# Kernel tuning notes

Hardware: AMD Instinct MI355X
Metric: run time of the kernel (lower is better)

The kernel has to match this reference:

```python
import jax, jax.numpy as jnp
import numpy as np

N_NODES = 50000


def _gcn_conv(x, edge_index, W, b):
    # PyG GCNConv (default flags): add self-loops, symmetric normalization,
    # linear transform, scatter-add aggregation, bias.
    N = x.shape[0]
    row, col = edge_index[0], edge_index[1]  # messages flow row -> col
    loop = jnp.arange(N)
    row_f = jnp.concatenate([row, loop])
    col_f = jnp.concatenate([col, loop])
    deg = jax.ops.segment_sum(jnp.ones(col_f.shape[0], dtype=x.dtype), col_f,
                              num_segments=N)
    deg_inv_sqrt = jnp.where(deg > 0, jax.lax.rsqrt(jnp.maximum(deg, 1e-12)), 0.0)
    norm = deg_inv_sqrt[row_f] * deg_inv_sqrt[col_f]  # [E+N]
    h = x @ W                                          # [N, out]
    msg = h[row_f] * norm[:, None]                     # gather + scale
    out = jax.ops.segment_sum(msg, col_f, num_segments=N)  # scatter-add
    return out + b


def setup_inputs() -> dict:
    key = jax.random.key(0)
    ks = jax.random.split(key, 6)
    d_in, d_hid, d_out = 128, 128, 64
    E = 800000
    x = jax.random.normal(ks[0], (N_NODES, d_in), dtype=jnp.float32)
    edge_index = jax.random.randint(ks[1], (2, E), 0, N_NODES, dtype=jnp.int64)
    edge_label = jax.random.uniform(ks[2], (100000,), dtype=jnp.float32)
    edge_label_index = jax.random.randint(ks[3], (2, 100000), 0, N_NODES,
                                          dtype=jnp.int64)
    # Glorot-style init for GCNConv linear weights
    W1 = jax.random.normal(ks[4], (d_in, d_hid), dtype=jnp.float32) / np.sqrt(d_in)
    b1 = jnp.zeros((d_hid,), dtype=jnp.float32)
    W2 = jax.random.normal(ks[5], (d_hid, d_out), dtype=jnp.float32) / np.sqrt(d_hid)
    b2 = jnp.zeros((d_out,), dtype=jnp.float32)
    return {"x": x, "edge_index": edge_index, "edge_label": edge_label,
            "edge_label_index": edge_label_index,
            "W1": W1, "b1": b1, "W2": W2, "b2": b2}


def reference(x, edge_index, edge_label, edge_label_index, W1, b1, W2, b2):
    h = jax.nn.relu(_gcn_conv(x, edge_index, W1, b1))
    # dropout is identity in eval mode (training=False)
    z = _gcn_conv(h, edge_index, W2, b2)
    return z
```

## Files before the change

### kernel.cpp

```cpp
#include <hip/hip_runtime.h>


typedef unsigned int u32;
typedef unsigned short ushort;
typedef __attribute__((ext_vector_type(8))) short short8;
typedef __attribute__((ext_vector_type(8))) unsigned short us8;
typedef __attribute__((ext_vector_type(4))) float floatx4;

static inline int cdiv_l(long a, int b) { return (int)((a + b - 1) / b); }

constexpr int NPB  = 512;
constexpr int EPB  = 4096;
constexpr int MAXB = 128;
constexpr int CAP  = 12288;

__device__ __forceinline__ u32 pack_bf16(float a, float b) {
  union { float f; u32 i; } ua, ub;
  ua.f = a; ub.f = b;
  u32 x = (ua.i + 0x7fffu + ((ua.i >> 16) & 1u)) >> 16;
  u32 y = (ub.i + 0x7fffu + ((ub.i >> 16) & 1u)) & 0xffff0000u;
  return x | y;
}

__device__ __forceinline__ short bf16r(float f) {
  union { float f; u32 i; } u; u.f = f;
  return (short)((u.i + 0x7fffu + ((u.i >> 16) & 1u)) >> 16);
}

__device__ __forceinline__ void dq8(float* a, uint2 v, float sd) {
  a[0] += (float)(v.x & 255u) * sd;
  a[1] += (float)((v.x >> 8) & 255u) * sd;
  a[2] += (float)((v.x >> 16) & 255u) * sd;
  a[3] += (float)(v.x >> 24) * sd;
  a[4] += (float)(v.y & 255u) * sd;
  a[5] += (float)((v.y >> 8) & 255u) * sd;
  a[6] += (float)((v.y >> 16) & 255u) * sd;
  a[7] += (float)(v.y >> 24) * sd;
}

__global__ __launch_bounds__(256) void k_pack(
    const float* __restrict__ W1, const float* __restrict__ W2,
    u32* __restrict__ w1f, u32* __restrict__ w2f, int* __restrict__ cur) {
  const int tid = threadIdx.x;
  const int b = blockIdx.x;
  if (b == 0 && tid < MAXB) cur[tid] = 0;
  if (b < 8) {
    const int s = b * 256 + tid;
    const int lane = s & 63, frag = s >> 6;
    const int kc = frag >> 3, cb = frag & 7;
    const float* src =
        W1 + (long)(kc * 32 + (lane >> 4) * 8) * 128 + cb * 16 + (lane & 15);
    u32 o[4];
#pragma unroll
    for (int p = 0; p < 4; ++p)
      o[p] = pack_bf16(src[(2 * p) * 128], src[(2 * p + 1) * 128]);
    *(uint4*)(w1f + (long)s * 4) = make_uint4(o[0], o[1], o[2], o[3]);
  } else {
    const int s = (b - 8) * 256 + tid;
    const int lane = s & 63, frag = s >> 6;
    const int kc = frag >> 2, cb = frag & 3;
    const float* src =
        W2 + (long)(kc * 32 + (lane >> 4) * 8) * 64 + cb * 16 + (lane & 15);
    u32 o[4];
#pragma unroll
    for (int p = 0; p < 4; ++p)
      o[p] = pack_bf16(src[(2 * p) * 64], src[(2 * p + 1) * 64]);
    *(uint4*)(w2f + (long)s * 4) = make_uint4(o[0], o[1], o[2], o[3]);
  }
}

__global__ __launch_bounds__(256) void k_fused1(
    const int* __restrict__ ei, int* __restrict__ cur, u32* __restrict__ ebuf,
    int E, int NBE,
    const float* __restrict__ x, const u32* __restrict__ w1f,
    u32* __restrict__ h8, float* __restrict__ scale, int N) {
  __shared__ float eb[4][16 * 133];
  const int tid = threadIdx.x;

  if (blockIdx.x < (unsigned)NBE) {
    u32* ecache = (u32*)&eb[0][0];
    int* hist   = (int*)&eb[2][0];
    int* curs   = hist + MAXB;
    const int* ecol = ei + E;
    if (tid < MAXB) hist[tid] = 0;
    __syncthreads();
    const int base = blockIdx.x * EPB;
#pragma unroll
    for (int j = 0; j < EPB / 256; ++j) {
      int e = base + j * 256 + tid;
      u32 pk = 0xffffffffu;
      if (e < E) {
        u32 r = (u32)ei[e];
        u32 c = (u32)ecol[e];
        pk = r | (c << 16);
        atomicAdd(hist + (c >> 9), 1);
      }
      ecache[j * 256 + tid] = pk;
    }
    __syncthreads();
    if (tid < MAXB) {
      int n = hist[tid];
      curs[tid] = tid * CAP + (n ? atomicAdd(cur + tid, n) : 0);
    }
    __syncthreads();
#pragma unroll
    for (int j = 0; j < EPB / 256; ++j) {
      u32 pk = ecache[j * 256 + tid];
      if (pk != 0xffffffffu) {
        u32 c = pk >> 16;
        int b = c >> 9;
        int p = atomicAdd(curs + b, 1);
        if (p < (b + 1) * CAP)
          ebuf[p] = (pk & 0xffffu) | ((c & (NPB - 1)) << 16);
      }
    }
    return;
  }

  constexpr int K = 128, NC = 8, LROW = 133;
  const int w = tid >> 6, lane = tid & 63;
  const int quad = lane >> 4, n16 = lane & 15;
  const int row0 = ((blockIdx.x - NBE) * 4 + w) * 16;

  floatx4 acc[NC];
#pragma unroll
  for (int c = 0; c < NC; ++c) acc[c] = {0.f, 0.f, 0.f, 0.f};

  const int am = row0 + n16;
  const bool av = am < N;
  const float* arow = x + (long)am * K;
  const short8* wf = (const short8*)w1f;

#pragma unroll
  for (int kc = 0; kc < 4; ++kc) {
    const int kb = kc * 32 + quad * 8;
    float4 a0 = make_float4(0.f, 0.f, 0.f, 0.f);
    float4 a1 = make_float4(0.f, 0.f, 0.f, 0.f);
    if (av) {
      a0 = *(const float4*)(arow + kb);
      a1 = *(const float4*)(arow + kb + 4);
    }
    short8 af;
    af[0] = bf16r(a0.x); af[1] = bf16r(a0.y); af[2] = bf16r(a0.z); af[3] = bf16r(a0.w);
    af[4] = bf16r(a1.x); af[5] = bf16r(a1.y); af[6] = bf16r(a1.z); af[7] = bf16r(a1.w);
#pragma unroll
    for (int c = 0; c < NC; ++c) {
      short8 bf = wf[(kc * 8 + c) * 64 + lane];
      acc[c] = __builtin_amdgcn_mfma_f32_16x16x32_bf16(af, bf, acc[c], 0, 0, 0);
    }
  }

  float* ep = eb[w];
#pragma unroll
  for (int c = 0; c < NC; ++c)
#pragma unroll
    for (int r = 0; r < 4; ++r)
      ep[(quad * 4 + r) * LROW + c * 16 + n16] = acc[c][r];
  __syncthreads();

  const int rr = lane >> 2, seg = lane & 3;
  const float* rowp = ep + rr * LROW + seg * 32;
  float m = 0.f;
#pragma unroll
  for (int c = 0; c < 32; ++c) m = fmaxf(m, fabsf(rowp[c]));
  m = fmaxf(m, __shfl_xor(m, 1, 4));
  m = fmaxf(m, __shfl_xor(m, 2, 4));
  const float inv = (m > 0.f) ? 127.f / m : 0.f;
  const float s = m / 127.f;
  u32 q[8];
#pragma unroll
  for (int wd = 0; wd < 8; ++wd) {
    u32 b0 = (u32)((int)rintf(rowp[wd * 4 + 0] * inv) + 128);
    u32 b1 = (u32)((int)rintf(rowp[wd * 4 + 1] * inv) + 128);
    u32 b2 = (u32)((int)rintf(rowp[wd * 4 + 2] * inv) + 128);
    u32 b3 = (u32)((int)rintf(rowp[wd * 4 + 3] * inv) + 128);
    q[wd] = (b0 & 255u) | ((b1 & 255u) << 8) | ((b2 & 255u) << 16) | (b3 << 24);
  }
  const int rg = row0 + rr;
  if (rg < N) {
    uint4* dst = (uint4*)(h8 + (long)rg * 32 + seg * 8);
    dst[0] = make_uint4(q[0], q[1], q[2], q[3]);
    dst[1] = make_uint4(q[4], q[5], q[6], q[7]);
    if (seg == 0) scale[rg] = s;
  }
}

__global__ __launch_bounds__(NPB) void k_csr(const u32* __restrict__ ebuf,
                                             const int* __restrict__ cur,
                                             const float* __restrict__ scale,
                                             int* __restrict__ off,
                                             int* __restrict__ deg,
                                             float* __restrict__ dis,
                                             float* __restrict__ sd,
                                             ushort* __restrict__ csr, int N) {
  __shared__ int cnt[NPB];
  __shared__ int curl[NPB];
  __shared__ int wsum[NPB / 64];
  const int tid = threadIdx.x;
  const int b = blockIdx.x;
  const int s = b * CAP;
  const int e = s + min(cur[b], CAP);
  cnt[tid] = 0;
  __syncthreads();
  for (int i = s + tid; i < e; i += NPB)
    atomicAdd(cnt + (ebuf[i] >> 16), 1);
  __syncthreads();
  const int lane = tid & 63, w = tid >> 6;
  const int v = cnt[tid];
  const int vp = (v + 7) & ~7;
  int incl = vp;
#pragma unroll
  for (int d = 1; d < 64; d <<= 1) {
    int x = __shfl_up(incl, d, 64);
    if (lane >= d) incl += x;
  }
  if (lane == 63) wsum[w] = incl;
  __syncthreads();
  if (w == 0 && lane < NPB / 64) {
    int sv = wsum[lane];
#pragma unroll
    for (int d = 1; d < NPB / 64; d <<= 1) {
      int x = __shfl_up(sv, d, 64);
      if (lane >= d) sv += x;
    }
    wsum[lane] = sv;
  }
  __syncthreads();
  int excl = ((w > 0) ? wsum[w - 1] : 0) + incl - vp;
  int node = b * NPB + tid;
  if (node < N) {
    float dv = rsqrtf((float)v + 1.0f);
    off[node] = s + excl;
    deg[node] = v;
    dis[node] = dv;
    sd[node] = scale[node] * dv;
  }
  curl[tid] = excl;
  __syncthreads();
  for (int i = s + tid; i < e; i += NPB) {
    u32 pk = ebuf[i];
    int p = atomicAdd(curl + (pk >> 16), 1);
    csr[s + p] = (ushort)(pk & 0xffffu);
  }
}

__global__ __launch_bounds__(256) void k_gg(
    const uint2* __restrict__ h8, const int* __restrict__ off,
    const int* __restrict__ deg, const ushort* __restrict__ csr,
    const float* __restrict__ dis, const float* __restrict__ sd,
    const float* __restrict__ b1, const u32* __restrict__ w2f,
    u32* __restrict__ h2, float* __restrict__ s2, int N) {
  constexpr int LG = 65;
  constexpr int LC = 66;
  __shared__ u32 lg[16 * LG];
  __shared__ float cb[16 * LC];
  const int tid = threadIdx.x;
  const int r = tid >> 4;
  const int lf = tid & 15;
  const int row0 = blockIdx.x * 16;
  const int n = row0 + r;

  u32 gw[4] = {0, 0, 0, 0};
  if (n < N) {
    const int s = off[n], e = s + deg[n];
    const float dn = dis[n];
    float acc[8] = {};
    float K = 0.f;
    {
      float sn = sd[n];
      dq8(acc, h8[(long)n * 16 + lf], sn);
      K += sn;
    }
    int j = s;
    for (; j + 8 <= e; j += 8) {
      us8 ev = *(const us8*)(csr + j);
      const int i0 = ev[0], i1 = ev[1], i2 = ev[2], i3 = ev[3];
      const int i4 = ev[4], i5 = ev[5], i6 = ev[6], i7 = ev[7];
      const float d0 = sd[i0], d1 = sd[i1], d2 = sd[i2], d3 = sd[i3];
      const float d4 = sd[i4], d5 = sd[i5], d6 = sd[i6], d7 = sd[i7];
      uint2 v0 = h8[(long)i0 * 16 + lf];
      uint2 v1 = h8[(long)i1 * 16 + lf];
      uint2 v2 = h8[(long)i2 * 16 + lf];
      uint2 v3 = h8[(long)i3 * 16 + lf];
      uint2 v4 = h8[(long)i4 * 16 + lf];
      uint2 v5 = h8[(long)i5 * 16 + lf];
      uint2 v6 = h8[(long)i6 * 16 + lf];
      uint2 v7 = h8[(long)i7 * 16 + lf];
      dq8(acc, v0, d0); dq8(acc, v1, d1); dq8(acc, v2, d2); dq8(acc, v3, d3);
      dq8(acc, v4, d4); dq8(acc, v5, d5); dq8(acc, v6, d6); dq8(acc, v7, d7);
      K += ((d0 + d1) + (d2 + d3)) + ((d4 + d5) + (d6 + d7));
    }
    if (j < e) {
      us8 ev = *(const us8*)(csr + j);
#pragma unroll
      for (int t = 0; t < 8; ++t) {
        if (j + t < e) {
          const int it = ev[t];
          const float dt = sd[it];
          dq8(acc, h8[(long)it * 16 + lf], dt);
          K += dt;
        }
      }
    }
    const int f8 = lf * 8;
    const float4 bv0 = *(const float4*)(b1 + f8);
    const float4 bv1 = *(const float4*)(b1 + f8 + 4);
    const float bb[8] = {bv0.x, bv0.y, bv0.z, bv0.w, bv1.x, bv1.y, bv1.z, bv1.w};
    const float kc = 128.f * K;
#pragma unroll
    for (int q = 0; q < 8; ++q)
      acc[q] = fmaxf((acc[q] - kc) * dn + bb[q], 0.f);
#pragma unroll
    for (int q = 0; q < 4; ++q)
      gw[q] = pack_bf16(acc[2 * q], acc[2 * q + 1]);
  }
#pragma unroll
  for (int q = 0; q < 4; ++q) lg[r * LG + lf * 4 + q] = gw[q];
  __syncthreads();

  const int w = tid >> 6, lane = tid & 63;
  const int quad = lane >> 4, n16 = lane & 15;
  floatx4 acc4 = {0.f, 0.f, 0.f, 0.f};
#pragma unroll
  for (int kc = 0; kc < 4; ++kc) {
    const int kb = kc * 32 + quad * 8;
    const u32* ap = &lg[n16 * LG + (kb >> 1)];
    u32 aw[4] = {ap[0], ap[1], ap[2], ap[3]};
    short8 af = *(short8*)aw;
    short8 bf = ((const short8*)w2f)[(kc * 4 + w) * 64 + lane];
    acc4 = __builtin_amdgcn_mfma_f32_16x16x32_bf16(af, bf, acc4, 0, 0, 0);
  }
  float dd[4];
#pragma unroll
  for (int r4 = 0; r4 < 4; ++r4) {
    int rg = row0 + quad * 4 + r4;
    dd[r4] = (rg < N) ? dis[rg] : 0.f;
  }
#pragma unroll
  for (int r4 = 0; r4 < 4; ++r4)
    cb[(quad * 4 + r4) * LC + w * 16 + n16] = acc4[r4] * dd[r4];
  __syncthreads();

  const int rr2 = tid >> 4, lf2 = tid & 15;
  const float* rp = cb + rr2 * LC + lf2 * 4;
  float mx = fmaxf(fmaxf(fabsf(rp[0]), fabsf(rp[1])),
                   fmaxf(fabsf(rp[2]), fabsf(rp[3])));
  mx = fmaxf(mx, __shfl_xor(mx, 1, 16));
  mx = fmaxf(mx, __shfl_xor(mx, 2, 16));
  mx = fmaxf(mx, __shfl_xor(mx, 4, 16));
  mx = fmaxf(mx, __shfl_xor(mx, 8, 16));
  const float inv2 = (mx > 0.f) ? 127.f / mx : 0.f;
  const int rg2 = row0 + rr2;
  if (rg2 < N) {
    u32 q0 = (u32)((int)rintf(rp[0] * inv2) + 128);
    u32 q1 = (u32)((int)rintf(rp[1] * inv2) + 128);
    u32 q2 = (u32)((int)rintf(rp[2] * inv2) + 128);
    u32 q3 = (u32)((int)rintf(rp[3] * inv2) + 128);
    h2[(long)rg2 * 16 + lf2] =
        (q0 & 255u) | ((q1 & 255u) << 8) | ((q2 & 255u) << 16) | (q3 << 24);
    if (lf2 == 0) s2[rg2] = mx / 127.f;
  }
}

__global__ __launch_bounds__(256) void k_gather2(
    const uint2* __restrict__ hs, const int* __restrict__ off,
    const int* __restrict__ deg, const ushort* __restrict__ csr,
    const float* __restrict__ dis, const float* __restrict__ sc2,
    const float* __restrict__ bias, float* __restrict__ out, int N) {
  constexpr int L = 8;
  const int local = threadIdx.x / L;
  const int lf = threadIdx.x % L;
  const int n = blockIdx.x * (256 / L) + local;
  if (n >= N) return;
  const int s = off[n], e = s + deg[n];
  float acc[8] = {};
  float K = 0.f;
  {
    float t0 = sc2[n];
    dq8(acc, hs[(long)n * L + lf], t0);
    K += t0;
  }
  int j = s;
  for (; j + 8 <= e; j += 8) {
    us8 ev = *(const us8*)(csr + j);
    const int i0 = ev[0], i1 = ev[1], i2 = ev[2], i3 = ev[3];
    const int i4 = ev[4], i5 = ev[5], i6 = ev[6], i7 = ev[7];
    const float d0 = sc2[i0], d1 = sc2[i1], d2 = sc2[i2], d3 = sc2[i3];
    const float d4 = sc2[i4], d5 = sc2[i5], d6 = sc2[i6], d7 = sc2[i7];
    uint2 v0 = hs[(long)i0 * L + lf];
    uint2 v1 = hs[(long)i1 * L + lf];
    uint2 v2 = hs[(long)i2 * L + lf];
    uint2 v3 = hs[(long)i3 * L + lf];
    uint2 v4 = hs[(long)i4 * L + lf];
    uint2 v5 = hs[(long)i5 * L + lf];
    uint2 v6 = hs[(long)i6 * L + lf];
    uint2 v7 = hs[(long)i7 * L + lf];
    dq8(acc, v0, d0); dq8(acc, v1, d1); dq8(acc, v2, d2); dq8(acc, v3, d3);
    dq8(acc, v4, d4); dq8(acc, v5, d5); dq8(acc, v6, d6); dq8(acc, v7, d7);
    K += ((d0 + d1) + (d2 + d3)) + ((d4 + d5) + (d6 + d7));
  }
  if (j < e) {
    us8 ev = *(const us8*)(csr + j);
#pragma unroll
    for (int t = 0; t < 8; ++t) {
      if (j + t < e) {
        const int it = ev[t];
        const float dt = sc2[it];
        dq8(acc, hs[(long)it * L + lf], dt);
        K += dt;
      }
    }
  }
  const float d = dis[n];
  const float kc = 128.f * K;
  const int f8 = lf * 8;
  const float4 b0 = *(const float4*)(bias + f8);
  const float4 b1v = *(const float4*)(bias + f8 + 4);
  float4 o0, o1;
  o0.x = (acc[0] - kc) * d + b0.x;
  o0.y = (acc[1] - kc) * d + b0.y;
  o0.z = (acc[2] - kc) * d + b0.z;
  o0.w = (acc[3] - kc) * d + b0.w;
  o1.x = (acc[4] - kc) * d + b1v.x;
  o1.y = (acc[5] - kc) * d + b1v.y;
  o1.z = (acc[6] - kc) * d + b1v.z;
  o1.w = (acc[7] - kc) * d + b1v.w;
  *(float4*)(out + (long)n * 64 + f8) = o0;
  *(float4*)(out + (long)n * 64 + f8 + 4) = o1;
}

extern "C" void kernel_launch(void* const* d_in, const int* in_sizes, int n_in,
                              void* d_out, int out_size, void* d_ws, size_t ws_size,
                              hipStream_t stream) {
  const float* x  = (const float*)d_in[0];
  const int*   ei = (const int*)d_in[1];
  const float* W1 = (const float*)d_in[4];
  const float* b1 = (const float*)d_in[5];
  const float* W2 = (const float*)d_in[6];
  const float* b2 = (const float*)d_in[7];
  float* out = (float*)d_out;

  const int N = in_sizes[0] / 128;
  const int E = in_sizes[1] / 2;
  const int NBKT = cdiv_l(N, NPB);
  const int NBE  = cdiv_l(E, EPB);
  const int G1   = cdiv_l(N, 64);

  const long Np = (N + 64) & ~63L;
  const long BW = (long)NBKT * CAP;
  int*    cur   = (int*)d_ws;
  int*    off   = cur + 128;
  int*    deg   = off + Np;
  float*  dis   = (float*)(deg + Np);
  float*  scale = dis + Np;
  float*  sd    = scale + Np;
  float*  s2    = sd + Np;
  u32*    w1f   = (u32*)(s2 + Np);
  u32*    w2f   = w1f + 8192;
  u32*    ebuf  = w2f + 4096;
  ushort* csr   = (ushort*)(ebuf + BW);
  u32*    h8    = (u32*)(csr + BW);
  u32*    h2    = h8 + (long)N * 32;

  k_pack<<<12, 256, 0, stream>>>(W1, W2, w1f, w2f, cur);

  k_fused1<<<NBE + G1, 256, 0, stream>>>(ei, cur, ebuf, E, NBE, x, w1f, h8,
                                         scale, N);

  k_csr<<<NBKT, NPB, 0, stream>>>(ebuf, cur, scale, off, deg, dis, sd, csr, N);

  k_gg<<<cdiv_l(N, 16), 256, 0, stream>>>((const uint2*)h8, off, deg, csr,
                                          dis, sd, b1, w2f, h2, s2, N);

  k_gather2<<<cdiv_l(N, 32), 256, 0, stream>>>((const uint2*)h2, off, deg, csr,
                                               dis, s2, b2, out, N);
}
```

Baseline: 152.1 us.

## Merge pack, partition/GEMM1 and CSR build into one cooperative persistent kernel

Replaces three separate kernel launches (weight pack, edge partition plus first GEMM, CSR build) with a single cooperative kernel that loops over tiles and uses grid-wide syncs between phases. The CSR step is reworked to use 256 threads handling two nodes each, so it shares block size and LDS with the other phases. The aim is to remove launch gaps and tail effects between the small early stages. In exchange it adds grid.sync cost, limits the grid to the resident block count, and may lose occupancy under the new launch bounds. A fallback path keeps separate launches if the cooperative launch fails.

```diff
diff --git a/kernel.cpp b/kernel.cpp
--- a/kernel.cpp
+++ b/kernel.cpp
@@ -1,5 +1,8 @@
 #include <hip/hip_runtime.h>
-
+#include <hip/hip_cooperative_groups.h>
+
+
+namespace cg = cooperative_groups;
 
 typedef unsigned int u32;
 typedef unsigned short ushort;
@@ -38,12 +41,11 @@
   a[7] += (float)(v.y >> 24) * sd;
 }
 
-__global__ __launch_bounds__(256) void k_pack(
-    const float* __restrict__ W1, const float* __restrict__ W2,
-    u32* __restrict__ w1f, u32* __restrict__ w2f, int* __restrict__ cur) {
-  const int tid = threadIdx.x;
-  const int b = blockIdx.x;
-  if (b == 0 && tid < MAXB) cur[tid] = 0;
+
+__device__ __forceinline__ void pack_tile(int b, const float* __restrict__ W1,
+                                          const float* __restrict__ W2,
+                                          u32* __restrict__ w1f,
+                                          u32* __restrict__ w2f, int tid) {
   if (b < 8) {
     const int s = b * 256 + tid;
     const int lane = s & 63, frag = s >> 6;
@@ -69,6 +71,219 @@
   }
 }
 
+__device__ __forceinline__ void partition_tile(
+    int u, const int* __restrict__ ei, int* __restrict__ cur,
+    u32* __restrict__ ebuf, int E, int tid, float (*eb)[16 * 133]) {
+  u32* ecache = (u32*)&eb[0][0];
+  int* hist   = (int*)&eb[2][0];
+  int* curs   = hist + MAXB;
+  const int* ecol = ei + E;
+  if (tid < MAXB) hist[tid] = 0;
+  __syncthreads();
+  const int base = u * EPB;
+#pragma unroll
+  for (int j = 0; j < EPB / 256; ++j) {
+    int e = base + j * 256 + tid;
+    u32 pk = 0xffffffffu;
+    if (e < E) {
+      u32 r = (u32)ei[e];
+      u32 c = (u32)ecol[e];
+      pk = r | (c << 16);
+      atomicAdd(hist + (c >> 9), 1);
+    }
+    ecache[j * 256 + tid] = pk;
+  }
+  __syncthreads();
+  if (tid < MAXB) {
+    int n = hist[tid];
+    curs[tid] = tid * CAP + (n ? atomicAdd(cur + tid, n) : 0);
+  }
+  __syncthreads();
+#pragma unroll
+  for (int j = 0; j < EPB / 256; ++j) {
+    u32 pk = ecache[j * 256 + tid];
+    if (pk != 0xffffffffu) {
+      u32 c = pk >> 16;
+      int b = c >> 9;
+      int p = atomicAdd(curs + b, 1);
+      if (p < (b + 1) * CAP)
+        ebuf[p] = (pk & 0xffffu) | ((c & (NPB - 1)) << 16);
+    }
+  }
+  __syncthreads();
+}
+
+__device__ __forceinline__ void gemm1_tile(
+    int t, const float* __restrict__ x, const u32* __restrict__ w1f,
+    u32* __restrict__ h8, float* __restrict__ scale, int N, int tid,
+    float (*eb)[16 * 133]) {
+  constexpr int K = 128, NC = 8, LROW = 133;
+  const int w = tid >> 6, lane = tid & 63;
+  const int quad = lane >> 4, n16 = lane & 15;
+  const int row0 = (t * 4 + w) * 16;
+
+  floatx4 acc[NC];
+#pragma unroll
+  for (int c = 0; c < NC; ++c) acc[c] = {0.f, 0.f, 0.f, 0.f};
+
+  const int am = row0 + n16;
+  const bool av = am < N;
+  const float* arow = x + (long)am * K;
+  const short8* wf = (const short8*)w1f;
+
+#pragma unroll
+  for (int kc = 0; kc < 4; ++kc) {
+    const int kb = kc * 32 + quad * 8;
+    float4 a0 = make_float4(0.f, 0.f, 0.f, 0.f);
+    float4 a1 = make_float4(0.f, 0.f, 0.f, 0.f);
+    if (av) {
+      a0 = *(const float4*)(arow + kb);
+      a1 = *(const float4*)(arow + kb + 4);
+    }
+    short8 af;
+    af[0] = bf16r(a0.x); af[1] = bf16r(a0.y); af[2] = bf16r(a0.z); af[3] = bf16r(a0.w);
+    af[4] = bf16r(a1.x); af[5] = bf16r(a1.y); af[6] = bf16r(a1.z); af[7] = bf16r(a1.w);
+#pragma unroll
+    for (int c = 0; c < NC; ++c) {
+      short8 bf = wf[(kc * 8 + c) * 64 + lane];
+      acc[c] = __builtin_amdgcn_mfma_f32_16x16x32_bf16(af, bf, acc[c], 0, 0, 0);
+    }
+  }
+
+  float* ep = eb[w];
+#pragma unroll
+  for (int c = 0; c < NC; ++c)
+#pragma unroll
+    for (int r = 0; r < 4; ++r)
+      ep[(quad * 4 + r) * LROW + c * 16 + n16] = acc[c][r];
+  __syncthreads();
+
+  const int rr = lane >> 2, seg = lane & 3;
+  const float* rowp = ep + rr * LROW + seg * 32;
+  float m = 0.f;
+#pragma unroll
+  for (int c = 0; c < 32; ++c) m = fmaxf(m, fabsf(rowp[c]));
+  m = fmaxf(m, __shfl_xor(m, 1, 4));
+  m = fmaxf(m, __shfl_xor(m, 2, 4));
+  const float inv = (m > 0.f) ? 127.f / m : 0.f;
+  const float s = m / 127.f;
+  u32 q[8];
+#pragma unroll
+  for (int wd = 0; wd < 8; ++wd) {
+    u32 b0 = (u32)((int)rintf(rowp[wd * 4 + 0] * inv) + 128);
+    u32 b1 = (u32)((int)rintf(rowp[wd * 4 + 1] * inv) + 128);
+    u32 b2 = (u32)((int)rintf(rowp[wd * 4 + 2] * inv) + 128);
+    u32 b3 = (u32)((int)rintf(rowp[wd * 4 + 3] * inv) + 128);
+    q[wd] = (b0 & 255u) | ((b1 & 255u) << 8) | ((b2 & 255u) << 16) | (b3 << 24);
+  }
+  const int rg = row0 + rr;
+  if (rg < N) {
+    uint4* dst = (uint4*)(h8 + (long)rg * 32 + seg * 8);
+    dst[0] = make_uint4(q[0], q[1], q[2], q[3]);
+    dst[1] = make_uint4(q[4], q[5], q[6], q[7]);
+    if (seg == 0) scale[rg] = s;
+  }
+  __syncthreads();
+}
+
+__device__ __forceinline__ void csr_tile(
+    int b, const u32* __restrict__ ebuf, const int* __restrict__ cur,
+    const float* __restrict__ scale, int* __restrict__ off,
+    int* __restrict__ deg, float* __restrict__ dis, float* __restrict__ sd,
+    ushort* __restrict__ csr, int N, int tid, float (*eb)[16 * 133]) {
+  int* cnt  = (int*)&eb[0][0];
+  int* curl = cnt + NPB;
+  int* wsum = curl + NPB;
+  const int s = b * CAP;
+  const int e = s + min(cur[b], CAP);
+  cnt[tid] = 0; cnt[tid + 256] = 0;
+  __syncthreads();
+  for (int i = s + tid; i < e; i += 256)
+    atomicAdd(cnt + (ebuf[i] >> 16), 1);
+  __syncthreads();
+  const int lane = tid & 63, w = tid >> 6;
+  const int v0 = cnt[2 * tid], v1 = cnt[2 * tid + 1];
+  const int vp0 = (v0 + 7) & ~7, vp1 = (v1 + 7) & ~7;
+  const int pair = vp0 + vp1;
+  int incl = pair;
+#pragma unroll
+  for (int d = 1; d < 64; d <<= 1) {
+    int x = __shfl_up(incl, d, 64);
+    if (lane >= d) incl += x;
+  }
+  if (lane == 63) wsum[w] = incl;
+  __syncthreads();
+  if (w == 0 && lane < 4) {
+    int sv = wsum[lane];
+#pragma unroll
+    for (int d = 1; d < 4; d <<= 1) {
+      int x = __shfl_up(sv, d, 64);
+      if (lane >= d) sv += x;
+    }
+    wsum[lane] = sv;
+  }
+  __syncthreads();
+  const int excl = ((w > 0) ? wsum[w - 1] : 0) + incl - pair;
+  const int n0 = b * NPB + 2 * tid, n1 = n0 + 1;
+  if (n0 < N) {
+    float dv = rsqrtf((float)v0 + 1.0f);
+    off[n0] = s + excl; deg[n0] = v0; dis[n0] = dv; sd[n0] = scale[n0] * dv;
+  }
+  if (n1 < N) {
+    float dv = rsqrtf((float)v1 + 1.0f);
+    off[n1] = s + excl + vp0; deg[n1] = v1; dis[n1] = dv; sd[n1] = scale[n1] * dv;
+  }
+  curl[2 * tid] = excl; curl[2 * tid + 1] = excl + vp0;
+  __syncthreads();
+  for (int i = s + tid; i < e; i += 256) {
+    u32 pk = ebuf[i];
+    int p = atomicAdd(curl + (pk >> 16), 1);
+    csr[s + p] = (ushort)(pk & 0xffffu);
+  }
+  __syncthreads();
+}
+
+
+struct M1 {
+  const int* ei; const float* x; const float* W1; const float* W2;
+  int* cur; u32* ebuf; u32* w1f; u32* w2f; u32* h8; float* scale;
+  int* off; int* deg; float* dis; float* sd; ushort* csrp;
+  int E, NBE, G1, NBKT, N;
+};
+
+__global__ __launch_bounds__(256, 4) void k_mega1(M1 m) {
+  __shared__ float eb[4][16 * 133];
+  cg::grid_group grid = cg::this_grid();
+  const int tid = threadIdx.x;
+  const int G = gridDim.x;
+
+  for (int t = blockIdx.x; t < 13; t += G) {
+    if (t < 12) pack_tile(t, m.W1, m.W2, m.w1f, m.w2f, tid);
+    else if (tid < MAXB) m.cur[tid] = 0;
+  }
+  grid.sync();
+
+  const int T1 = m.NBE + m.G1;
+  for (int t = blockIdx.x; t < T1; t += G) {
+    if (t < m.NBE) partition_tile(t, m.ei, m.cur, m.ebuf, m.E, tid, eb);
+    else gemm1_tile(t - m.NBE, m.x, m.w1f, m.h8, m.scale, m.N, tid, eb);
+  }
+  grid.sync();
+
+  for (int t = blockIdx.x; t < m.NBKT; t += G)
+    csr_tile(t, m.ebuf, m.cur, m.scale, m.off, m.deg, m.dis, m.sd, m.csrp,
+             m.N, tid, eb);
+}
+
+
+__global__ __launch_bounds__(256) void k_pack(
+    const float* __restrict__ W1, const float* __restrict__ W2,
+    u32* __restrict__ w1f, u32* __restrict__ w2f, int* __restrict__ cur) {
+  const int tid = threadIdx.x;
+  if (blockIdx.x == 0 && tid < MAXB) cur[tid] = 0;
+  pack_tile(blockIdx.x, W1, W2, w1f, w2f, tid);
+}
+
 __global__ __launch_bounds__(256) void k_fused1(
     const int* __restrict__ ei, int* __restrict__ cur, u32* __restrict__ ebuf,
     int E, int NBE,
@@ -76,172 +291,20 @@
     u32* __restrict__ h8, float* __restrict__ scale, int N) {
   __shared__ float eb[4][16 * 133];
   const int tid = threadIdx.x;
-
-  if (blockIdx.x < (unsigned)NBE) {
-    u32* ecache = (u32*)&eb[0][0];
-    int* hist   = (int*)&eb[2][0];
-    int* curs   = hist + MAXB;
-    const int* ecol = ei + E;
-    if (tid < MAXB) hist[tid] = 0;
-    __syncthreads();
-    const int base = blockIdx.x * EPB;
-#pragma unroll
-    for (int j = 0; j < EPB / 256; ++j) {
-      int e = base + j * 256 + tid;
-      u32 pk = 0xffffffffu;
-      if (e < E) {
-        u32 r = (u32)ei[e];
-        u32 c = (u32)ecol[e];
-        pk = r | (c << 16);
-        atomicAdd(hist + (c >> 9), 1);
-      }
-      ecache[j * 256 + tid] = pk;
-    }
-    __syncthreads();
-    if (tid < MAXB) {
-      int n = hist[tid];
-      curs[tid] = tid * CAP + (n ? atomicAdd(cur + tid, n) : 0);
-    }
-    __syncthreads();
-#pragma unroll
-    for (int j = 0; j < EPB / 256; ++j) {
-      u32 pk = ecache[j * 256 + tid];
-      if (pk != 0xffffffffu) {
-        u32 c = pk >> 16;
-        int b = c >> 9;
-        int p = atomicAdd(curs + b, 1);
-        if (p < (b + 1) * CAP)
-          ebuf[p] = (pk & 0xffffu) | ((c & (NPB - 1)) << 16);
-      }
-    }
-    return;
-  }
-
-  constexpr int K = 128, NC = 8, LROW = 133;
-  const int w = tid >> 6, lane = tid & 63;
-  const int quad = lane >> 4, n16 = lane & 15;
-  const int row0 = ((blockIdx.x - NBE) * 4 + w) * 16;
-
-  floatx4 acc[NC];
-#pragma unroll
-  for (int c = 0; c < NC; ++c) acc[c] = {0.f, 0.f, 0.f, 0.f};
-
-  const int am = row0 + n16;
-  const bool av = am < N;
-  const float* arow = x + (long)am * K;
-  const short8* wf = (const short8*)w1f;
-
-#pragma unroll
-  for (int kc = 0; kc < 4; ++kc) {
-    const int kb = kc * 32 + quad * 8;
-    float4 a0 = make_float4(0.f, 0.f, 0.f, 0.f);
-    float4 a1 = make_float4(0.f, 0.f, 0.f, 0.f);
-    if (av) {
-      a0 = *(const float4*)(arow + kb);
-      a1 = *(const float4*)(arow + kb + 4);
-    }
-    short8 af;
-    af[0] = bf16r(a0.x); af[1] = bf16r(a0.y); af[2] = bf16r(a0.z); af[3] = bf16r(a0.w);
-    af[4] = bf16r(a1.x); af[5] = bf16r(a1.y); af[6] = bf16r(a1.z); af[7] = bf16r(a1.w);
-#pragma unroll
-    for (int c = 0; c < NC; ++c) {
-      short8 bf = wf[(kc * 8 + c) * 64 + lane];
-      acc[c] = __builtin_amdgcn_mfma_f32_16x16x32_bf16(af, bf, acc[c], 0, 0, 0);
-    }
-  }
-
-  float* ep = eb[w];
-#pragma unroll
-  for (int c = 0; c < NC; ++c)
-#pragma unroll
-    for (int r = 0; r < 4; ++r)
-      ep[(quad * 4 + r) * LROW + c * 16 + n16] = acc[c][r];
-  __syncthreads();
-
-  const int rr = lane >> 2, seg = lane & 3;
-  const float* rowp = ep + rr * LROW + seg * 32;
-  float m = 0.f;
-#pragma unroll
-  for (int c = 0; c < 32; ++c) m = fmaxf(m, fabsf(rowp[c]));
-  m = fmaxf(m, __shfl_xor(m, 1, 4));
-  m = fmaxf(m, __shfl_xor(m, 2, 4));
-  const float inv = (m > 0.f) ? 127.f / m : 0.f;
-  const float s = m / 127.f;
-  u32 q[8];
-#pragma unroll
-  for (int wd = 0; wd < 8; ++wd) {
-    u32 b0 = (u32)((int)rintf(rowp[wd * 4 + 0] * inv) + 128);
-    u32 b1 = (u32)((int)rintf(rowp[wd * 4 + 1] * inv) + 128);
-    u32 b2 = (u32)((int)rintf(rowp[wd * 4 + 2] * inv) + 128);
-    u32 b3 = (u32)((int)rintf(rowp[wd * 4 + 3] * inv) + 128);
-    q[wd] = (b0 & 255u) | ((b1 & 255u) << 8) | ((b2 & 255u) << 16) | (b3 << 24);
-  }
-  const int rg = row0 + rr;
-  if (rg < N) {
-    uint4* dst = (uint4*)(h8 + (long)rg * 32 + seg * 8);
-    dst[0] = make_uint4(q[0], q[1], q[2], q[3]);
-    dst[1] = make_uint4(q[4], q[5], q[6], q[7]);
-    if (seg == 0) scale[rg] = s;
-  }
-}
-
-__global__ __launch_bounds__(NPB) void k_csr(const u32* __restrict__ ebuf,
-                                             const int* __restrict__ cur,
-                                             const float* __restrict__ scale,
-                                             int* __restrict__ off,
-                                             int* __restrict__ deg,
-                                             float* __restrict__ dis,
-                                             float* __restrict__ sd,
-                                             ushort* __restrict__ csr, int N) {
-  __shared__ int cnt[NPB];
-  __shared__ int curl[NPB];
-  __shared__ int wsum[NPB / 64];
-  const int tid = threadIdx.x;
-  const int b = blockIdx.x;
-  const int s = b * CAP;
-  const int e = s + min(cur[b], CAP);
-  cnt[tid] = 0;
-  __syncthreads();
-  for (int i = s + tid; i < e; i += NPB)
-    atomicAdd(cnt + (ebuf[i] >> 16), 1);
-  __syncthreads();
-  const int lane = tid & 63, w = tid >> 6;
-  const int v = cnt[tid];
-  const int vp = (v + 7) & ~7;
-  int incl = vp;
-#pragma unroll
-  for (int d = 1; d < 64; d <<= 1) {
-    int x = __shfl_up(incl, d, 64);
-    if (lane >= d) incl += x;
-  }
-  if (lane == 63) wsum[w] = incl;
-  __syncthreads();
-  if (w == 0 && lane < NPB / 64) {
-    int sv = wsum[lane];
-#pragma unroll
-    for (int d = 1; d < NPB / 64; d <<= 1) {
-      int x = __shfl_up(sv, d, 64);
-      if (lane >= d) sv += x;
-    }
-    wsum[lane] = sv;
-  }
-  __syncthreads();
-  int excl = ((w > 0) ? wsum[w - 1] : 0) + incl - vp;
-  int node = b * NPB + tid;
-  if (node < N) {
-    float dv = rsqrtf((float)v + 1.0f);
-    off[node] = s + excl;
-    deg[node] = v;
-    dis[node] = dv;
-    sd[node] = scale[node] * dv;
-  }
-  curl[tid] = excl;
-  __syncthreads();
-  for (int i = s + tid; i < e; i += NPB) {
-    u32 pk = ebuf[i];
-    int p = atomicAdd(curl + (pk >> 16), 1);
-    csr[s + p] = (ushort)(pk & 0xffffu);
-  }
+  if (blockIdx.x < (unsigned)NBE)
+    partition_tile(blockIdx.x, ei, cur, ebuf, E, tid, eb);
+  else
+    gemm1_tile(blockIdx.x - NBE, x, w1f, h8, scale, N, tid, eb);
+}
+
+__global__ __launch_bounds__(256) void k_csr2(
+    const u32* __restrict__ ebuf, const int* __restrict__ cur,
+    const float* __restrict__ scale, int* __restrict__ off,
+    int* __restrict__ deg, float* __restrict__ dis, float* __restrict__ sd,
+    ushort* __restrict__ csr, int N) {
+  __shared__ float eb[4][16 * 133];
+  csr_tile(blockIdx.x, ebuf, cur, scale, off, deg, dis, sd, csr, N,
+           threadIdx.x, eb);
 }
 
 __global__ __launch_bounds__(256) void k_gg(
@@ -462,12 +525,40 @@
   u32*    h8    = (u32*)(csr + BW);
   u32*    h2    = h8 + (long)N * 32;
 
-  k_pack<<<12, 256, 0, stream>>>(W1, W2, w1f, w2f, cur);
-
-  k_fused1<<<NBE + G1, 256, 0, stream>>>(ei, cur, ebuf, E, NBE, x, w1f, h8,
-                                         scale, N);
-
-  k_csr<<<NBKT, NPB, 0, stream>>>(ebuf, cur, scale, off, deg, dis, sd, csr, N);
+  static int g_grid = -2;
+  if (g_grid == -2) {
+    int bpc = 0;
+    if (hipOccupancyMaxActiveBlocksPerMultiprocessor(
+            &bpc, (const void*)k_mega1, 256, 0) != hipSuccess)
+      bpc = 0;
+    int ncu = 0;
+    hipDeviceProp_t prop{};
+    int dev = 0;
+    hipGetDevice(&dev);
+    if (hipGetDeviceProperties(&prop, dev) == hipSuccess)
+      ncu = prop.multiProcessorCount;
+    g_grid = (bpc > 0 && ncu > 0) ? bpc * ncu : -1;
+  }
+
+  bool coop_ok = false;
+  if (g_grid > 0) {
+    M1 m;
+    m.ei = ei; m.x = x; m.W1 = W1; m.W2 = W2;
+    m.cur = cur; m.ebuf = ebuf; m.w1f = w1f; m.w2f = w2f;
+    m.h8 = h8; m.scale = scale;
+    m.off = off; m.deg = deg; m.dis = dis; m.sd = sd; m.csrp = csr;
+    m.E = E; m.NBE = NBE; m.G1 = G1; m.NBKT = NBKT; m.N = N;
+    void* kp[] = {(void*)&m};
+    coop_ok = hipLaunchCooperativeKernel((const void*)k_mega1, dim3(g_grid),
+                                         dim3(256), kp, 0, stream) == hipSuccess;
+  }
+  if (!coop_ok) {
+    k_pack<<<12, 256, 0, stream>>>(W1, W2, w1f, w2f, cur);
+    k_fused1<<<NBE + G1, 256, 0, stream>>>(ei, cur, ebuf, E, NBE, x, w1f, h8,
+                                           scale, N);
+    k_csr2<<<NBKT, 256, 0, stream>>>(ebuf, cur, scale, off, deg, dis, sd, csr,
+                                     N);
+  }
 
   k_gg<<<cdiv_l(N, 16), 256, 0, stream>>>((const uint2*)h8, off, deg, csr,
                                           dis, sd, b1, w2f, h2, s2, N);
```

Result: slower. 301.1 us (+98.0%).

## Pad CSR rows to multiples of eight with dummy node and unroll gathers by 16

Applied to the files above, without the earlier changes.

The CSR build now fills each node's padded slots (up to the next multiple of eight) with a dummy index N, whose scale entries sd[N] and s2[N] are zeroed in the pack kernel. Both gather kernels can then drop the per-element guarded tail and process whole groups of eight, with the main loop unrolled to sixteen neighbours per iteration for more memory-level parallelism. Padded edges read row N of h8/h2 but multiply by zero scale, adding a few wasted loads and relying on the layout reserving that row. Higher register use from the wider unroll may reduce occupancy.

```diff
diff --git a/kernel.cpp b/kernel.cpp
--- a/kernel.cpp
+++ b/kernel.cpp
@@ -40,10 +40,14 @@
 
 __global__ __launch_bounds__(256) void k_pack(
     const float* __restrict__ W1, const float* __restrict__ W2,
-    u32* __restrict__ w1f, u32* __restrict__ w2f, int* __restrict__ cur) {
+    u32* __restrict__ w1f, u32* __restrict__ w2f, int* __restrict__ cur,
+    float* __restrict__ sd, float* __restrict__ s2, int N) {
   const int tid = threadIdx.x;
   const int b = blockIdx.x;
-  if (b == 0 && tid < MAXB) cur[tid] = 0;
+  if (b == 0) {
+    if (tid < MAXB) cur[tid] = 0;
+    if (tid == 255) { sd[N] = 0.f; s2[N] = 0.f; }
+  }
   if (b < 8) {
     const int s = b * 256 + tid;
     const int lane = s & 63, frag = s >> 6;
@@ -236,6 +240,7 @@
     sd[node] = scale[node] * dv;
   }
   curl[tid] = excl;
+  for (int p = excl + v; p < excl + vp; ++p) csr[s + p] = (ushort)N;
   __syncthreads();
   for (int i = s + tid; i < e; i += NPB) {
     u32 pk = ebuf[i];
@@ -262,7 +267,8 @@
 
   u32 gw[4] = {0, 0, 0, 0};
   if (n < N) {
-    const int s = off[n], e = s + deg[n];
+    const int s = off[n];
+    const int ep = s + ((deg[n] + 7) & ~7);
     const float dn = dis[n];
     float acc[8] = {};
     float K = 0.f;
@@ -272,7 +278,41 @@
       K += sn;
     }
     int j = s;
-    for (; j + 8 <= e; j += 8) {
+    for (; j + 16 <= ep; j += 16) {
+      us8 ev0 = *(const us8*)(csr + j);
+      us8 ev1 = *(const us8*)(csr + j + 8);
+      const int i0 = ev0[0], i1 = ev0[1], i2 = ev0[2], i3 = ev0[3];
+      const int i4 = ev0[4], i5 = ev0[5], i6 = ev0[6], i7 = ev0[7];
+      const int i8 = ev1[0], i9 = ev1[1], ia = ev1[2], ib = ev1[3];
+      const int ic = ev1[4], id = ev1[5], ie = ev1[6], if_ = ev1[7];
+      const float d0 = sd[i0], d1 = sd[i1], d2 = sd[i2], d3 = sd[i3];
+      const float d4 = sd[i4], d5 = sd[i5], d6 = sd[i6], d7 = sd[i7];
+      const float d8 = sd[i8], d9 = sd[i9], da = sd[ia], db = sd[ib];
+      const float dc = sd[ic], dd_ = sd[id], de = sd[ie], df = sd[if_];
+      uint2 v0 = h8[(long)i0 * 16 + lf];
+      uint2 v1 = h8[(long)i1 * 16 + lf];
+      uint2 v2 = h8[(long)i2 * 16 + lf];
+      uint2 v3 = h8[(long)i3 * 16 + lf];
+      uint2 v4 = h8[(long)i4 * 16 + lf];
+      uint2 v5 = h8[(long)i5 * 16 + lf];
+      uint2 v6 = h8[(long)i6 * 16 + lf];
+      uint2 v7 = h8[(long)i7 * 16 + lf];
+      uint2 v8 = h8[(long)i8 * 16 + lf];
+      uint2 v9 = h8[(long)i9 * 16 + lf];
+      uint2 va = h8[(long)ia * 16 + lf];
+      uint2 vb = h8[(long)ib * 16 + lf];
+      uint2 vc = h8[(long)ic * 16 + lf];
+      uint2 vd = h8[(long)id * 16 + lf];
+      uint2 ve = h8[(long)ie * 16 + lf];
+      uint2 vf = h8[(long)if_ * 16 + lf];
+      dq8(acc, v0, d0); dq8(acc, v1, d1); dq8(acc, v2, d2); dq8(acc, v3, d3);
+      dq8(acc, v4, d4); dq8(acc, v5, d5); dq8(acc, v6, d6); dq8(acc, v7, d7);
+      dq8(acc, v8, d8); dq8(acc, v9, d9); dq8(acc, va, da); dq8(acc, vb, db);
+      dq8(acc, vc, dc); dq8(acc, vd, dd_); dq8(acc, ve, de); dq8(acc, vf, df);
+      K += (((d0 + d1) + (d2 + d3)) + ((d4 + d5) + (d6 + d7))) +
+           (((d8 + d9) + (da + db)) + ((dc + dd_) + (de + df)));
+    }
+    if (j < ep) {
       us8 ev = *(const us8*)(csr + j);
       const int i0 = ev[0], i1 = ev[1], i2 = ev[2], i3 = ev[3];
       const int i4 = ev[4], i5 = ev[5], i6 = ev[6], i7 = ev[7];
@@ -289,18 +329,6 @@
       dq8(acc, v0, d0); dq8(acc, v1, d1); dq8(acc, v2, d2); dq8(acc, v3, d3);
       dq8(acc, v4, d4); dq8(acc, v5, d5); dq8(acc, v6, d6); dq8(acc, v7, d7);
       K += ((d0 + d1) + (d2 + d3)) + ((d4 + d5) + (d6 + d7));
-    }
-    if (j < e) {
-      us8 ev = *(const us8*)(csr + j);
-#pragma unroll
-      for (int t = 0; t < 8; ++t) {
-        if (j + t < e) {
-          const int it = ev[t];
-          const float dt = sd[it];
-          dq8(acc, h8[(long)it * 16 + lf], dt);
-          K += dt;
-        }
-      }
     }
     const int f8 = lf * 8;
     const float4 bv0 = *(const float4*)(b1 + f8);
@@ -372,7 +400,8 @@
   const int lf = threadIdx.x % L;
   const int n = blockIdx.x * (256 / L) + local;
   if (n >= N) return;
-  const int s = off[n], e = s + deg[n];
+  const int s = off[n];
+  const int ep = s + ((deg[n] + 7) & ~7);
   float acc[8] = {};
   float K = 0.f;
   {
@@ -381,7 +410,41 @@
     K += t0;
   }
   int j = s;
-  for (; j + 8 <= e; j += 8) {
+  for (; j + 16 <= ep; j += 16) {
+    us8 ev0 = *(const us8*)(csr + j);
+    us8 ev1 = *(const us8*)(csr + j + 8);
+    const int i0 = ev0[0], i1 = ev0[1], i2 = ev0[2], i3 = ev0[3];
+    const int i4 = ev0[4], i5 = ev0[5], i6 = ev0[6], i7 = ev0[7];
+    const int i8 = ev1[0], i9 = ev1[1], ia = ev1[2], ib = ev1[3];
+    const int ic = ev1[4], id = ev1[5], ie = ev1[6], if_ = ev1[7];
+    const float d0 = sc2[i0], d1 = sc2[i1], d2 = sc2[i2], d3 = sc2[i3];
+    const float d4 = sc2[i4], d5 = sc2[i5], d6 = sc2[i6], d7 = sc2[i7];
+    const float d8 = sc2[i8], d9 = sc2[i9], da = sc2[ia], db = sc2[ib];
+    const float dc = sc2[ic], dd_ = sc2[id], de = sc2[ie], df = sc2[if_];
+    uint2 v0 = hs[(long)i0 * L + lf];
+    uint2 v1 = hs[(long)i1 * L + lf];
+    uint2 v2 = hs[(long)i2 * L + lf];
+    uint2 v3 = hs[(long)i3 * L + lf];
+    uint2 v4 = hs[(long)i4 * L + lf];
+    uint2 v5 = hs[(long)i5 * L + lf];
+    uint2 v6 = hs[(long)i6 * L + lf];
+    uint2 v7 = hs[(long)i7 * L + lf];
+    uint2 v8 = hs[(long)i8 * L + lf];
+    uint2 v9 = hs[(long)i9 * L + lf];
+    uint2 va = hs[(long)ia * L + lf];
+    uint2 vb = hs[(long)ib * L + lf];
+    uint2 vc = hs[(long)ic * L + lf];
+    uint2 vd = hs[(long)id * L + lf];
+    uint2 ve = hs[(long)ie * L + lf];
+    uint2 vf = hs[(long)if_ * L + lf];
+    dq8(acc, v0, d0); dq8(acc, v1, d1); dq8(acc, v2, d2); dq8(acc, v3, d3);
+    dq8(acc, v4, d4); dq8(acc, v5, d5); dq8(acc, v6, d6); dq8(acc, v7, d7);
+    dq8(acc, v8, d8); dq8(acc, v9, d9); dq8(acc, va, da); dq8(acc, vb, db);
+    dq8(acc, vc, dc); dq8(acc, vd, dd_); dq8(acc, ve, de); dq8(acc, vf, df);
+    K += (((d0 + d1) + (d2 + d3)) + ((d4 + d5) + (d6 + d7))) +
+         (((d8 + d9) + (da + db)) + ((dc + dd_) + (de + df)));
+  }
+  if (j < ep) {
     us8 ev = *(const us8*)(csr + j);
     const int i0 = ev[0], i1 = ev[1], i2 = ev[2], i3 = ev[3];
     const int i4 = ev[4], i5 = ev[5], i6 = ev[6], i7 = ev[7];
@@ -399,18 +462,6 @@
     dq8(acc, v4, d4); dq8(acc, v5, d5); dq8(acc, v6, d6); dq8(acc, v7, d7);
     K += ((d0 + d1) + (d2 + d3)) + ((d4 + d5) + (d6 + d7));
   }
-  if (j < e) {
-    us8 ev = *(const us8*)(csr + j);
-#pragma unroll
-    for (int t = 0; t < 8; ++t) {
-      if (j + t < e) {
-        const int it = ev[t];
-        const float dt = sc2[it];
-        dq8(acc, hs[(long)it * L + lf], dt);
-        K += dt;
-      }
-    }
-  }
   const float d = dis[n];
   const float kc = 128.f * K;
   const int f8 = lf * 8;
@@ -462,7 +513,7 @@
   u32*    h8    = (u32*)(csr + BW);
   u32*    h2    = h8 + (long)N * 32;
 
-  k_pack<<<12, 256, 0, stream>>>(W1, W2, w1f, w2f, cur);
+  k_pack<<<12, 256, 0, stream>>>(W1, W2, w1f, w2f, cur, sd, s2, N);
 
   k_fused1<<<NBE + G1, 256, 0, stream>>>(ei, cur, ebuf, E, NBE, x, w1f, h8,
                                          scale, N);
```

After: 156.1 us. +2.7%, slower.

## Merge weight packing into front kernel and replace global bucket atomics with per-chunk slots

Applied to the files above, without the earlier changes.

Removes the separate k_pack launch. W1 is now converted to bf16 inline inside the GEMM blocks, and W2 packing runs as four extra blocks of the front kernel. The global atomic bucket cursor is replaced by fixed per-chunk sub-slots (SUBCAP=80) with a per-chunk histogram, and k_csr scans all slots and filters them by that histogram. This saves one launch and the zeroing dependency. In exchange, k_csr scans padded slots with an integer divide per element, the GEMM now does redundant strided W1 loads, and edges are silently dropped if more than 80 land in one bucket from a chunk.

```diff
diff --git a/kernel.cpp b/kernel.cpp
--- a/kernel.cpp
+++ b/kernel.cpp
@@ -9,10 +9,11 @@
 
 static inline int cdiv_l(long a, int b) { return (int)((a + b - 1) / b); }
 
-constexpr int NPB  = 512;
-constexpr int EPB  = 4096;
-constexpr int MAXB = 128;
-constexpr int CAP  = 12288;
+constexpr int NPB    = 512;
+constexpr int EPB    = 4096;
+constexpr int MAXB   = 128;
+constexpr int SUBCAP = 80;
+constexpr int CAPW   = 16384;
 
 __device__ __forceinline__ u32 pack_bf16(float a, float b) {
   union { float f; u32 i; } ua, ub;
@@ -38,25 +39,18 @@
   a[7] += (float)(v.y >> 24) * sd;
 }
 
-__global__ __launch_bounds__(256) void k_pack(
-    const float* __restrict__ W1, const float* __restrict__ W2,
-    u32* __restrict__ w1f, u32* __restrict__ w2f, int* __restrict__ cur) {
+__global__ __launch_bounds__(256) void k_front(
+    const int* __restrict__ ei, u32* __restrict__ ebuf,
+    int* __restrict__ histg, int E, int NBE, int G1,
+    const float* __restrict__ x, const float* __restrict__ W1,
+    const float* __restrict__ W2, u32* __restrict__ w2f,
+    u32* __restrict__ h8, float* __restrict__ scale, int N) {
+  __shared__ float eb[4][16 * 133];
   const int tid = threadIdx.x;
-  const int b = blockIdx.x;
-  if (b == 0 && tid < MAXB) cur[tid] = 0;
-  if (b < 8) {
-    const int s = b * 256 + tid;
-    const int lane = s & 63, frag = s >> 6;
-    const int kc = frag >> 3, cb = frag & 7;
-    const float* src =
-        W1 + (long)(kc * 32 + (lane >> 4) * 8) * 128 + cb * 16 + (lane & 15);
-    u32 o[4];
-#pragma unroll
-    for (int p = 0; p < 4; ++p)
-      o[p] = pack_bf16(src[(2 * p) * 128], src[(2 * p + 1) * 128]);
-    *(uint4*)(w1f + (long)s * 4) = make_uint4(o[0], o[1], o[2], o[3]);
-  } else {
-    const int s = (b - 8) * 256 + tid;
+  const int blk = blockIdx.x;
+
+  if (blk >= NBE + G1) {
+    const int s = (blk - NBE - G1) * 256 + tid;
     const int lane = s & 63, frag = s >> 6;
     const int kc = frag >> 2, cb = frag & 3;
     const float* src =
@@ -66,25 +60,17 @@
     for (int p = 0; p < 4; ++p)
       o[p] = pack_bf16(src[(2 * p) * 64], src[(2 * p + 1) * 64]);
     *(uint4*)(w2f + (long)s * 4) = make_uint4(o[0], o[1], o[2], o[3]);
-  }
-}
-
-__global__ __launch_bounds__(256) void k_fused1(
-    const int* __restrict__ ei, int* __restrict__ cur, u32* __restrict__ ebuf,
-    int E, int NBE,
-    const float* __restrict__ x, const u32* __restrict__ w1f,
-    u32* __restrict__ h8, float* __restrict__ scale, int N) {
-  __shared__ float eb[4][16 * 133];
-  const int tid = threadIdx.x;
-
-  if (blockIdx.x < (unsigned)NBE) {
+    return;
+  }
+
+  if (blk < NBE) {
     u32* ecache = (u32*)&eb[0][0];
     int* hist   = (int*)&eb[2][0];
     int* curs   = hist + MAXB;
     const int* ecol = ei + E;
-    if (tid < MAXB) hist[tid] = 0;
+    if (tid < MAXB) { hist[tid] = 0; curs[tid] = 0; }
     __syncthreads();
-    const int base = blockIdx.x * EPB;
+    const int base = blk * EPB;
 #pragma unroll
     for (int j = 0; j < EPB / 256; ++j) {
       int e = base + j * 256 + tid;
@@ -98,10 +84,7 @@
       ecache[j * 256 + tid] = pk;
     }
     __syncthreads();
-    if (tid < MAXB) {
-      int n = hist[tid];
-      curs[tid] = tid * CAP + (n ? atomicAdd(cur + tid, n) : 0);
-    }
+    if (tid < MAXB) histg[blk * MAXB + tid] = min(hist[tid], SUBCAP);
     __syncthreads();
 #pragma unroll
     for (int j = 0; j < EPB / 256; ++j) {
@@ -110,17 +93,18 @@
         u32 c = pk >> 16;
         int b = c >> 9;
         int p = atomicAdd(curs + b, 1);
-        if (p < (b + 1) * CAP)
-          ebuf[p] = (pk & 0xffffu) | ((c & (NPB - 1)) << 16);
+        if (p < SUBCAP)
+          ebuf[(long)b * (NBE * SUBCAP) + blk * SUBCAP + p] =
+              (pk & 0xffffu) | ((c & (NPB - 1)) << 16);
       }
     }
     return;
   }
 
-  constexpr int K = 128, NC = 8, LROW = 133;
+  constexpr int K = 128, M = 128, NC = 8, LROW = 133;
   const int w = tid >> 6, lane = tid & 63;
   const int quad = lane >> 4, n16 = lane & 15;
-  const int row0 = ((blockIdx.x - NBE) * 4 + w) * 16;
+  const int row0 = ((blk - NBE) * 4 + w) * 16;
 
   floatx4 acc[NC];
 #pragma unroll
@@ -129,7 +113,6 @@
   const int am = row0 + n16;
   const bool av = am < N;
   const float* arow = x + (long)am * K;
-  const short8* wf = (const short8*)w1f;
 
 #pragma unroll
   for (int kc = 0; kc < 4; ++kc) {
@@ -143,9 +126,15 @@
     short8 af;
     af[0] = bf16r(a0.x); af[1] = bf16r(a0.y); af[2] = bf16r(a0.z); af[3] = bf16r(a0.w);
     af[4] = bf16r(a1.x); af[5] = bf16r(a1.y); af[6] = bf16r(a1.z); af[7] = bf16r(a1.w);
+    const float* wbase = W1 + (long)kb * M + n16;
 #pragma unroll
     for (int c = 0; c < NC; ++c) {
-      short8 bf = wf[(kc * 8 + c) * 64 + lane];
+      const float* wp = wbase + c * 16;
+      short8 bf;
+      bf[0] = bf16r(wp[0 * M]); bf[1] = bf16r(wp[1 * M]);
+      bf[2] = bf16r(wp[2 * M]); bf[3] = bf16r(wp[3 * M]);
+      bf[4] = bf16r(wp[4 * M]); bf[5] = bf16r(wp[5 * M]);
+      bf[6] = bf16r(wp[6 * M]); bf[7] = bf16r(wp[7 * M]);
       acc[c] = __builtin_amdgcn_mfma_f32_16x16x32_bf16(af, bf, acc[c], 0, 0, 0);
     }
   }
@@ -186,24 +175,29 @@
 }
 
 __global__ __launch_bounds__(NPB) void k_csr(const u32* __restrict__ ebuf,
-                                             const int* __restrict__ cur,
+                                             const int* __restrict__ histg,
                                              const float* __restrict__ scale,
                                              int* __restrict__ off,
                                              int* __restrict__ deg,
                                              float* __restrict__ dis,
                                              float* __restrict__ sd,
-                                             ushort* __restrict__ csr, int N) {
+                                             ushort* __restrict__ csr,
+                                             int NBE, int N) {
   __shared__ int cnt[NPB];
   __shared__ int curl[NPB];
   __shared__ int wsum[NPB / 64];
   const int tid = threadIdx.x;
   const int b = blockIdx.x;
-  const int s = b * CAP;
-  const int e = s + min(cur[b], CAP);
+  const int TOT = NBE * SUBCAP;
+  const long ebase = (long)b * TOT;
   cnt[tid] = 0;
   __syncthreads();
-  for (int i = s + tid; i < e; i += NPB)
-    atomicAdd(cnt + (ebuf[i] >> 16), 1);
+  for (int i = tid; i < TOT; i += NPB) {
+    const int chunk = i / SUBCAP;
+    const int pos = i - chunk * SUBCAP;
+    if (pos < histg[chunk * MAXB + b])
+      atomicAdd(cnt + (ebuf[ebase + i] >> 16), 1);
+  }
   __syncthreads();
   const int lane = tid & 63, w = tid >> 6;
   const int v = cnt[tid];
@@ -226,21 +220,26 @@
     wsum[lane] = sv;
   }
   __syncthreads();
-  int excl = ((w > 0) ? wsum[w - 1] : 0) + incl - vp;
-  int node = b * NPB + tid;
+  const int excl = ((w > 0) ? wsum[w - 1] : 0) + incl - vp;
+  const int node = b * NPB + tid;
   if (node < N) {
     float dv = rsqrtf((float)v + 1.0f);
-    off[node] = s + excl;
+    off[node] = b * CAPW + excl;
     deg[node] = v;
     dis[node] = dv;
     sd[node] = scale[node] * dv;
   }
   curl[tid] = excl;
   __syncthreads();
-  for (int i = s + tid; i < e; i += NPB) {
-    u32 pk = ebuf[i];
-    int p = atomicAdd(curl + (pk >> 16), 1);
-    csr[s + p] = (ushort)(pk & 0xffffu);
+  ushort* cw = csr + (long)b * CAPW;
+  for (int i = tid; i < TOT; i += NPB) {
+    const int chunk = i / SUBCAP;
+    const int pos = i - chunk * SUBCAP;
+    if (pos < histg[chunk * MAXB + b]) {
+      u32 pk = ebuf[ebase + i];
+      int p = atomicAdd(curl + (pk >> 16), 1);
+      cw[p] = (ushort)(pk & 0xffffu);
+    }
   }
 }
 
@@ -445,29 +444,27 @@
   const int NBKT = cdiv_l(N, NPB);
   const int NBE  = cdiv_l(E, EPB);
   const int G1   = cdiv_l(N, 64);
+  const int CAPB = NBE * SUBCAP;
 
   const long Np = (N + 64) & ~63L;
-  const long BW = (long)NBKT * CAP;
-  int*    cur   = (int*)d_ws;
-  int*    off   = cur + 128;
+  int*    histg = (int*)d_ws;
+  int*    off   = histg + (long)NBE * MAXB;
   int*    deg   = off + Np;
   float*  dis   = (float*)(deg + Np);
   float*  scale = dis + Np;
   float*  sd    = scale + Np;
   float*  s2    = sd + Np;
-  u32*    w1f   = (u32*)(s2 + Np);
-  u32*    w2f   = w1f + 8192;
+  u32*    w2f   = (u32*)(s2 + Np);
   u32*    ebuf  = w2f + 4096;
-  ushort* csr   = (ushort*)(ebuf + BW);
-  u32*    h8    = (u32*)(csr + BW);
+  ushort* csr   = (ushort*)(ebuf + (long)NBKT * CAPB);
+  u32*    h8    = (u32*)(csr + (long)NBKT * CAPW);
   u32*    h2    = h8 + (long)N * 32;
 
-  k_pack<<<12, 256, 0, stream>>>(W1, W2, w1f, w2f, cur);
-
-  k_fused1<<<NBE + G1, 256, 0, stream>>>(ei, cur, ebuf, E, NBE, x, w1f, h8,
-                                         scale, N);
-
-  k_csr<<<NBKT, NPB, 0, stream>>>(ebuf, cur, scale, off, deg, dis, sd, csr, N);
+  k_front<<<NBE + G1 + 4, 256, 0, stream>>>(ei, ebuf, histg, E, NBE, G1, x,
+                                            W1, W2, w2f, h8, scale, N);
+
+  k_csr<<<NBKT, NPB, 0, stream>>>(ebuf, histg, scale, off, deg, dis, sd, csr,
+                                  NBE, N);
 
   k_gg<<<cdiv_l(N, 16), 256, 0, stream>>>((const uint2*)h8, off, deg, csr,
                                           dis, sd, b1, w2f, h2, s2, N);
```

Result: slower. 167.3 us (+10.0%).
